# Performance work log

Measured on AMD Instinct MI355X. Metric: run time of the kernel, lower is better.

## Reference

```python
import jax, jax.numpy as jnp
import numpy as np

HIDDEN = 768
HEADS = 12
HEAD_DIM = HIDDEN // HEADS
INTER = 1152
WINDOW = 128
EPS = 1e-5
ROPE_WAVELENGTH = 10000.0


def setup_inputs() -> dict:
    key = jax.random.key(0)
    ks = jax.random.split(key, 8)
    B, S = 2, 2048
    x = jax.random.normal(ks[0], (B, S, HIDDEN), dtype=jnp.float32)
    padding_mask = jnp.ones((B, S), dtype=jnp.int32)
    sc = 0.02
    wqkv = jax.random.normal(ks[1], (HIDDEN, 3 * HIDDEN), dtype=jnp.float32) * sc
    wo_attn = jax.random.normal(ks[2], (HIDDEN, HIDDEN), dtype=jnp.float32) * sc
    wi0 = jax.random.normal(ks[3], (HIDDEN, INTER), dtype=jnp.float32) * sc
    wi1 = jax.random.normal(ks[4], (HIDDEN, INTER), dtype=jnp.float32) * sc
    wo_mlp = jax.random.normal(ks[5], (INTER, HIDDEN), dtype=jnp.float32) * sc
    g_attn = jnp.ones((HIDDEN,), dtype=jnp.float32)
    g_mlp = jnp.ones((HIDDEN,), dtype=jnp.float32)
    return dict(x=x, padding_mask=padding_mask, wqkv=wqkv, wo_attn=wo_attn,
                wi0=wi0, wi1=wi1, wo_mlp=wo_mlp, g_attn=g_attn, g_mlp=g_mlp)


def _rmsnorm(x, gamma):
    # Keras LayerNormalization(rms_scaling=True): x * rsqrt(mean(x^2)+eps) * gamma
    inv = jax.lax.rsqrt(jnp.mean(jnp.square(x), axis=-1, keepdims=True) + EPS)
    return x * inv * gamma


def _rope(t):
    # t: [B, S, H, D]; standard rotate-half RoPE over the head dim
    S, D = t.shape[1], t.shape[3]
    inv_freq = 1.0 / (ROPE_WAVELENGTH ** (jnp.arange(0, D, 2, dtype=jnp.float32) / D))
    freqs = jnp.arange(S, dtype=jnp.float32)[:, None] * inv_freq[None, :]  # [S, D/2]
    emb = jnp.concatenate([freqs, freqs], axis=-1)  # [S, D]
    cos = jnp.cos(emb)[None, :, None, :]
    sin = jnp.sin(emb)[None, :, None, :]
    h1, h2 = jnp.split(t, 2, axis=-1)
    rot = jnp.concatenate([-h2, h1], axis=-1)
    return t * cos + rot * sin


def reference(x, padding_mask, wqkv, wo_attn, wi0, wi1, wo_mlp, g_attn, g_mlp):
    B, S, _ = x.shape
    # --- attention sub-block ---
    res = x
    h = _rmsnorm(x, g_attn)
    qkv = (h @ wqkv).reshape(B, S, 3, HEADS, HEAD_DIM)
    q, k, v = qkv[:, :, 0], qkv[:, :, 1], qkv[:, :, 2]  # [B, S, H, D]
    q = _rope(q)
    k = _rope(k)
    scores = jnp.einsum('bqhd,bkhd->bhqk', q, k) / jnp.sqrt(
        jnp.asarray(HEAD_DIM, x.dtype))
    pos = jnp.arange(S)
    window = (jnp.abs(pos[:, None] - pos[None, :]) <= WINDOW // 2).astype(jnp.float32)
    mask = window[None, None, :, :] * padding_mask.astype(jnp.float32)[:, None, None, :]
    scores = scores + (1.0 - mask) * -1e9
    attn = jax.nn.softmax(scores, axis=-1)
    out = jnp.einsum('bhqk,bkhd->bqhd', attn, v).reshape(B, S, HIDDEN)
    x = res + out @ wo_attn
    # --- GeGLU MLP sub-block ---
    res = x
    h = _rmsnorm(x, g_mlp)
    h = jax.nn.gelu(h @ wi0, approximate=True) * (h @ wi1)
    return res + h @ wo_mlp
```

## Files before the change

### kernel.cpp

```cpp
#include <hip/hip_runtime.h>
#include <hip/hip_bf16.h>

#define HID 768
#define NHEADS 12
#define HD 64
#define INTER 1152
#define SEQ 2048
#define NB 2
#define ROWS (NB * SEQ)
#define QTA 64
#define KTA 192

typedef __attribute__((ext_vector_type(8))) short bf16x8;
typedef __attribute__((ext_vector_type(4))) float f32x4;

__device__ __forceinline__ float bf2f(unsigned short u) {
    union { unsigned int i; float f; } c; c.i = ((unsigned int)u) << 16; return c.f;
}
__device__ __forceinline__ unsigned short f2bf(float f) {
    union { float f; unsigned int i; } c; c.f = f;
    unsigned int b = c.i;
    b += 0x7FFFu + ((b >> 16) & 1u);
    return (unsigned short)(b >> 16);
}
__device__ __forceinline__ void gload16(const void* g, void* l) {
    __builtin_amdgcn_global_load_lds((const __attribute__((address_space(1))) unsigned int*)g,
                                     (__attribute__((address_space(3))) unsigned int*)l,
                                     16, 0, 0);
}

__global__ __launch_bounds__(256) void rmsnorm_kernel(const float* __restrict__ x,
                                                      const float* __restrict__ g,
                                                      unsigned short* __restrict__ out) {
    int row = blockIdx.x;
    const float* xr = x + (size_t)row * HID;
    unsigned short* orow = out + (size_t)row * HID;
    int tid = threadIdx.x;
    float v0 = xr[tid], v1 = xr[tid + 256], v2 = xr[tid + 512];
    float s = v0 * v0 + v1 * v1 + v2 * v2;
    #pragma unroll
    for (int m = 32; m >= 1; m >>= 1) s += __shfl_xor(s, m, 64);
    __shared__ float red[4];
    if ((tid & 63) == 0) red[tid >> 6] = s;
    __syncthreads();
    float tot = red[0] + red[1] + red[2] + red[3];
    float inv = rsqrtf(tot * (1.0f / HID) + 1e-5f);
    orow[tid]       = f2bf(v0 * inv * g[tid]);
    orow[tid + 256] = f2bf(v1 * inv * g[tid + 256]);
    orow[tid + 512] = f2bf(v2 * inv * g[tid + 512]);
}

__device__ __forceinline__ void wt_tile(const float* __restrict__ W,
                                        unsigned short* __restrict__ Wt,
                                        int K, int N, int bx, int by,
                                        float (*t)[33]) {
    int tx = threadIdx.x & 31, ty = threadIdx.x >> 5;
    #pragma unroll
    for (int i = 0; i < 4; ++i)
        t[ty + i * 8][tx] = W[(size_t)(by * 32 + ty + i * 8) * N + bx * 32 + tx];
    __syncthreads();
    #pragma unroll
    for (int i = 0; i < 4; ++i)
        Wt[(size_t)(bx * 32 + ty + i * 8) * K + by * 32 + tx] = f2bf(t[tx][ty + i * 8]);
}

__global__ __launch_bounds__(256) void prep_kernel(const float* __restrict__ wqkv,
                                                   const float* __restrict__ woa,
                                                   const float* __restrict__ wi0,
                                                   const float* __restrict__ wi1,
                                                   const float* __restrict__ wom,
                                                   unsigned short* __restrict__ wqkvT,
                                                   unsigned short* __restrict__ woaT,
                                                   unsigned short* __restrict__ wi0T,
                                                   unsigned short* __restrict__ wi1T,
                                                   unsigned short* __restrict__ womT,
                                                   float2* __restrict__ rtab) {
    __shared__ float t[32][33];
    int id = blockIdx.x;
    if (id < 1728)       wt_tile(wqkv, wqkvT, 768, 2304, id % 72, id / 72, t);
    else if (id < 2304)  { id -= 1728; wt_tile(woa, woaT, 768, 768, id % 24, id / 24, t); }
    else if (id < 3168)  { id -= 2304; wt_tile(wi0, wi0T, 768, 1152, id % 36, id / 36, t); }
    else if (id < 4032)  { id -= 3168; wt_tile(wi1, wi1T, 768, 1152, id % 36, id / 36, t); }
    else if (id < 4896)  { id -= 4032; wt_tile(wom, womT, 1152, 768, id % 24, id / 24, t); }
    else {
        int idx = (id - 4896) * 256 + threadIdx.x;
        int s = idx >> 5, fi = idx & 31;
        float ang = (float)s * exp2f(-(float)fi * 0.41524101186f);
        float sn, cs;
        sincosf(ang, &sn, &cs);
        rtab[idx] = make_float2(cs, sn);
    }
}

__global__ __launch_bounds__(256) void mfma_gemm64(const unsigned short* __restrict__ A,
                                                   const unsigned short* __restrict__ Bt,
                                                   const float* __restrict__ resid,
                                                   float* __restrict__ C,
                                                   int N, int K, int nbx) {
    __shared__ unsigned short As[64 * 64];
    __shared__ unsigned short Bs[64 * 64];
    int nwg = gridDim.x;
    int bid = blockIdx.x;
    int id2 = (bid & 7) * (nwg >> 3) + (bid >> 3);
    int row0 = (id2 / nbx) * 64, col0 = (id2 % nbx) * 64;
    int tid = threadIdx.x;
    int wave = tid >> 6, lane = tid & 63;
    int wr = wave >> 1, wc = wave & 1;
    int fr = lane & 15, fq = lane >> 4;

    f32x4 acc[2][2];
    #pragma unroll
    for (int m = 0; m < 2; ++m)
        #pragma unroll
        for (int n = 0; n < 2; ++n)
            acc[m][n] = (f32x4){0.f, 0.f, 0.f, 0.f};

    const size_t strideA = (size_t)K * 2;
    const char* Ab = (const char*)A;
    const char* Bb = (const char*)Bt;

    for (int k0 = 0; k0 < K; k0 += 64) {
        #pragma unroll
        for (int r = 0; r < 2; ++r) {
            int L = r * 4096 + tid * 16;
            int row = L >> 7;
            int ss = ((L >> 4) & 7) ^ (row & 7);
            gload16(Ab + (size_t)(row0 + row) * strideA + (size_t)k0 * 2 + ss * 16,
                    (char*)As + L);
            gload16(Bb + (size_t)(col0 + row) * strideA + (size_t)k0 * 2 + ss * 16,
                    (char*)Bs + L);
        }
        __syncthreads();
        bf16x8 af[2][2], bff[2][2];
        #pragma unroll
        for (int m = 0; m < 2; ++m)
            #pragma unroll
            for (int kk = 0; kk < 2; ++kk) {
                int rowa = wr * 32 + m * 16 + fr;
                af[m][kk] = *(const bf16x8*)&As[rowa * 64 + ((kk * 4 + fq) ^ (rowa & 7)) * 8];
                int rowb = wc * 32 + m * 16 + fr;
                bff[m][kk] = *(const bf16x8*)&Bs[rowb * 64 + ((kk * 4 + fq) ^ (rowb & 7)) * 8];
            }
        #pragma unroll
        for (int m = 0; m < 2; ++m)
            #pragma unroll
            for (int n = 0; n < 2; ++n) {
                acc[m][n] = __builtin_amdgcn_mfma_f32_16x16x32_bf16(af[m][0], bff[n][0], acc[m][n], 0, 0, 0);
                acc[m][n] = __builtin_amdgcn_mfma_f32_16x16x32_bf16(af[m][1], bff[n][1], acc[m][n], 0, 0, 0);
            }
        __syncthreads();
    }

    #pragma unroll
    for (int m = 0; m < 2; ++m) {
        #pragma unroll
        for (int j = 0; j < 4; ++j) {
            size_t r = (size_t)(row0 + wr * 32 + m * 16 + fq * 4 + j);
            #pragma unroll
            for (int n = 0; n < 2; ++n) {
                size_t idx = r * N + (col0 + wc * 32 + n * 16 + fr);
                float v = acc[m][n][j];
                if (resid) v += resid[idx];
                C[idx] = v;
            }
        }
    }
}

__global__ __launch_bounds__(256) void gemm_qkv128(const unsigned short* __restrict__ A,
                                                   const unsigned short* __restrict__ Bt,
                                                   const float2* __restrict__ rtab,
                                                   unsigned short* __restrict__ Qb,
                                                   unsigned short* __restrict__ Kb,
                                                   unsigned short* __restrict__ Vt) {
    __shared__ unsigned short As[128 * 64];
    __shared__ unsigned short Bs[64 * 64];
    int bid = blockIdx.x;
    int id2 = (bid & 7) * 144 + (bid >> 3);
    int col0 = (id2 % 36) * 64, row0 = (id2 / 36) * 128;
    int tid = threadIdx.x;
    int wave = tid >> 6, lane = tid & 63;
    int fr = lane & 15, fq = lane >> 4;
    int type = col0 / 768;
    int h = (col0 % 768) >> 6;
    int b = row0 >> 11;
    int s0 = row0 & 2047;
    int bh = b * NHEADS + h;

    f32x4 acc[2][4];
    #pragma unroll
    for (int m = 0; m < 2; ++m)
        #pragma unroll
        for (int n = 0; n < 4; ++n)
            acc[m][n] = (f32x4){0.f, 0.f, 0.f, 0.f};

    const size_t strideA = (size_t)768 * 2;
    const char* Ab = (const char*)A;
    const char* Bb = (const char*)Bt;

    for (int k0 = 0; k0 < 768; k0 += 64) {
        #pragma unroll
        for (int r = 0; r < 4; ++r) {
            int L = r * 4096 + tid * 16;
            int row = L >> 7;
            int ss = ((L >> 4) & 7) ^ (row & 7);
            gload16(Ab + (size_t)(row0 + row) * strideA + (size_t)k0 * 2 + ss * 16,
                    (char*)As + L);
        }
        #pragma unroll
        for (int r = 0; r < 2; ++r) {
            int L = r * 4096 + tid * 16;
            int row = L >> 7;
            int ss = ((L >> 4) & 7) ^ (row & 7);
            gload16(Bb + (size_t)(col0 + row) * strideA + (size_t)k0 * 2 + ss * 16,
                    (char*)Bs + L);
        }
        __syncthreads();
        #pragma unroll
        for (int kk = 0; kk < 2; ++kk) {
            bf16x8 af[2], bf[4];
            #pragma unroll
            for (int m = 0; m < 2; ++m) {
                int rowa = wave * 32 + m * 16 + fr;
                af[m] = *(const bf16x8*)&As[rowa * 64 + ((kk * 4 + fq) ^ (rowa & 7)) * 8];
            }
            #pragma unroll
            for (int n = 0; n < 4; ++n) {
                int rowb = n * 16 + fr;
                bf[n] = *(const bf16x8*)&Bs[rowb * 64 + ((kk * 4 + fq) ^ (rowb & 7)) * 8];
            }
            #pragma unroll
            for (int m = 0; m < 2; ++m)
                #pragma unroll
                for (int n = 0; n < 4; ++n)
                    acc[m][n] = __builtin_amdgcn_mfma_f32_16x16x32_bf16(af[m], bf[n], acc[m][n], 0, 0, 0);
        }
        __syncthreads();
    }

    if (type < 2) {
        unsigned short* P = (type == 0 ? Qb : Kb) + ((size_t)bh * SEQ) * 64;
        #pragma unroll
        for (int m = 0; m < 2; ++m)
            #pragma unroll
            for (int n = 0; n < 4; ++n) {
                int d = n * 16 + fr;
                int fi = d & 31;
                #pragma unroll
                for (int j = 0; j < 4; ++j) {
                    int s = s0 + wave * 32 + m * 16 + fq * 4 + j;
                    float2 cs = rtab[s * 32 + fi];
                    float val = acc[m][n][j], par = acc[m][n ^ 2][j];
                    float o = (d < 32) ? val * cs.x - par * cs.y
                                       : val * cs.x + par * cs.y;
                    P[(size_t)s * 64 + d] = f2bf(o);
                }
            }
    } else {
        unsigned short* vt = As;
        #pragma unroll
        for (int m = 0; m < 2; ++m)
            #pragma unroll
            for (int n = 0; n < 4; ++n) {
                int d = n * 16 + fr;
                #pragma unroll
                for (int j = 0; j < 4; ++j)
                    vt[d * 136 + wave * 32 + m * 16 + fq * 4 + j] = f2bf(acc[m][n][j]);
            }
        __syncthreads();
        int d = tid >> 2, sg = tid & 3;
        unsigned short* vrow = Vt + ((size_t)bh * 64 + d) * SEQ + s0 + sg * 32;
        #pragma unroll
        for (int i = 0; i < 4; ++i)
            *(bf16x8*)(vrow + i * 8) = *(const bf16x8*)&vt[d * 136 + sg * 32 + i * 8];
    }
}

__global__ __launch_bounds__(256) void gemm_ffn128(const unsigned short* __restrict__ A,
                                                   const unsigned short* __restrict__ B0t,
                                                   const unsigned short* __restrict__ B1t,
                                                   unsigned short* __restrict__ O) {
    __shared__ unsigned short As[128 * 64];
    __shared__ unsigned short Bs0[64 * 64];
    __shared__ unsigned short Bs1[64 * 64];
    int bid = blockIdx.x;
    int id2 = (bid & 7) * 72 + (bid >> 3);
    int col0 = (id2 % 18) * 64, row0 = (id2 / 18) * 128;
    int tid = threadIdx.x;
    int wave = tid >> 6, lane = tid & 63;
    int fr = lane & 15, fq = lane >> 4;

    f32x4 acc0[2][4], acc1[2][4];
    #pragma unroll
    for (int m = 0; m < 2; ++m)
        #pragma unroll
        for (int n = 0; n < 4; ++n) {
            acc0[m][n] = (f32x4){0.f, 0.f, 0.f, 0.f};
            acc1[m][n] = (f32x4){0.f, 0.f, 0.f, 0.f};
        }

    const size_t strideA = (size_t)768 * 2;
    const char* Ab  = (const char*)A;
    const char* B0b = (const char*)B0t;
    const char* B1b = (const char*)B1t;

    for (int k0 = 0; k0 < 768; k0 += 64) {
        #pragma unroll
        for (int r = 0; r < 4; ++r) {
            int L = r * 4096 + tid * 16;
            int row = L >> 7;
            int ss = ((L >> 4) & 7) ^ (row & 7);
            gload16(Ab + (size_t)(row0 + row) * strideA + (size_t)k0 * 2 + ss * 16,
                    (char*)As + L);
        }
        #pragma unroll
        for (int r = 0; r < 2; ++r) {
            int L = r * 4096 + tid * 16;
            int row = L >> 7;
            int ss = ((L >> 4) & 7) ^ (row & 7);
            size_t goff = (size_t)(col0 + row) * strideA + (size_t)k0 * 2 + ss * 16;
            gload16(B0b + goff, (char*)Bs0 + L);
            gload16(B1b + goff, (char*)Bs1 + L);
        }
        __syncthreads();
        #pragma unroll
        for (int kk = 0; kk < 2; ++kk) {
            bf16x8 af[2], b0[4], b1[4];
            #pragma unroll
            for (int m = 0; m < 2; ++m) {
                int rowa = wave * 32 + m * 16 + fr;
                af[m] = *(const bf16x8*)&As[rowa * 64 + ((kk * 4 + fq) ^ (rowa & 7)) * 8];
            }
            #pragma unroll
            for (int n = 0; n < 4; ++n) {
                int rowb = n * 16 + fr;
                int sl = ((kk * 4 + fq) ^ (rowb & 7)) * 8;
                b0[n] = *(const bf16x8*)&Bs0[rowb * 64 + sl];
                b1[n] = *(const bf16x8*)&Bs1[rowb * 64 + sl];
            }
            #pragma unroll
            for (int m = 0; m < 2; ++m)
                #pragma unroll
                for (int n = 0; n < 4; ++n) {
                    acc0[m][n] = __builtin_amdgcn_mfma_f32_16x16x32_bf16(af[m], b0[n], acc0[m][n], 0, 0, 0);
                    acc1[m][n] = __builtin_amdgcn_mfma_f32_16x16x32_bf16(af[m], b1[n], acc1[m][n], 0, 0, 0);
                }
        }
        __syncthreads();
    }

    #pragma unroll
    for (int m = 0; m < 2; ++m)
        #pragma unroll
        for (int n = 0; n < 4; ++n)
            #pragma unroll
            for (int j = 0; j < 4; ++j) {
                int r = row0 + wave * 32 + m * 16 + fq * 4 + j;
                float xa = acc0[m][n][j];
                float tn = tanhf(0.7978845608028654f * (xa + 0.044715f * xa * xa * xa));
                float gv = 0.5f * xa * (1.f + tn) * acc1[m][n][j];
                O[(size_t)r * INTER + col0 + n * 16 + fr] = f2bf(gv);
            }
}

__global__ __launch_bounds__(256) void attn_mfma(const unsigned short* __restrict__ Qb,
                                                 const unsigned short* __restrict__ Kb,
                                                 const unsigned short* __restrict__ Vt,
                                                 const int* __restrict__ pmask,
                                                 unsigned short* __restrict__ ao) {
    __shared__ unsigned short Ks[KTA * 64];
    __shared__ unsigned short Vs[64 * KTA];
    __shared__ unsigned short Ps[4][16 * KTA];
    __shared__ float pmsk[KTA];

    int bid = blockIdx.x;
    int qt = bid & 31;
    int h  = (bid >> 5) % NHEADS;
    int b  = bid / (32 * NHEADS);
    int bh = b * NHEADS + h;
    int q0 = qt * QTA;
    int kstart = q0 - 64;
    int tid = threadIdx.x;
    int wave = tid >> 6, lane = tid & 63;
    int fr = lane & 15, fq = lane >> 4;

    const unsigned short* Kg = Kb + ((size_t)bh * SEQ) * 64;
    const unsigned short* Vg = Vt + ((size_t)bh * 64) * SEQ;

    if (tid < KTA) {
        int k = kstart + tid;
        pmsk[tid] = (k >= 0 && k < SEQ) ? (1.0f - (float)pmask[b * SEQ + k]) * -1e9f
                                        : -1e9f;
    }

    bool interior = (qt != 0) && (qt != 31);
    if (interior) {
        #pragma unroll
        for (int r = 0; r < 6; ++r) {
            int c = r * 256 + tid;
            int row = c >> 3, slot = c & 7;
            int ss = slot ^ (row & 7);
            gload16(Kg + (size_t)(kstart + row) * 64 + ss * 8, (char*)Ks + c * 16);
        }
        #pragma unroll
        for (int r = 0; r < 6; ++r) {
            int c = r * 256 + tid;
            int d = c / 24, slot = c - d * 24;
            int ss = (slot & ~7) | ((slot & 7) ^ (d & 7));
            gload16(Vg + (size_t)d * SEQ + kstart + ss * 8, (char*)Vs + c * 16);
        }
    } else {
        #pragma unroll
        for (int r = 0; r < 6; ++r) {
            int c = r * 256 + tid;
            int row = c >> 3, slot = c & 7;
            int ss = slot ^ (row & 7);
            int sk = kstart + row;
            bf16x8 val = {0, 0, 0, 0, 0, 0, 0, 0};
            if (sk >= 0 && sk < SEQ)
                val = *(const bf16x8*)(Kg + (size_t)sk * 64 + ss * 8);
            *(bf16x8*)((char*)Ks + c * 16) = val;
        }
        #pragma unroll
        for (int r = 0; r < 6; ++r) {
            int c = r * 256 + tid;
            int d = c / 24, slot = c - d * 24;
            int ss = (slot & ~7) | ((slot & 7) ^ (d & 7));
            int start = kstart + ss * 8;
            bf16x8 val = {0, 0, 0, 0, 0, 0, 0, 0};
            if (start >= 0 && start + 8 <= SEQ)
                val = *(const bf16x8*)(Vg + (size_t)d * SEQ + start);
            *(bf16x8*)((char*)Vs + c * 16) = val;
        }
    }
    __syncthreads();

    const unsigned short* Qg = Qb + ((size_t)bh * SEQ + q0 + wave * 16 + fr) * 64 + fq * 8;
    bf16x8 qf0 = *(const bf16x8*)(Qg);
    bf16x8 qf1 = *(const bf16x8*)(Qg + 32);

    f32x4 sc[12];
    #pragma unroll
    for (int n = 0; n < 12; ++n) sc[n] = (f32x4){0.f, 0.f, 0.f, 0.f};
    #pragma unroll
    for (int n = 0; n < 12; ++n) {
        int row = n * 16 + fr;
        int base = row * 64;
        bf16x8 k0 = *(const bf16x8*)&Ks[base + ((fq)     ^ (row & 7)) * 8];
        bf16x8 k1 = *(const bf16x8*)&Ks[base + ((4 + fq) ^ (row & 7)) * 8];
        sc[n] = __builtin_amdgcn_mfma_f32_16x16x32_bf16(qf0, k0, sc[n], 0, 0, 0);
        sc[n] = __builtin_amdgcn_mfma_f32_16x16x32_bf16(qf1, k1, sc[n], 0, 0, 0);
    }

    int qrow_base = q0 + wave * 16 + fq * 4;
    float mj[4] = {-1e30f, -1e30f, -1e30f, -1e30f}, sj[4];
    #pragma unroll
    for (int n = 0; n < 12; ++n) {
        int k = kstart + n * 16 + fr;
        float pm = pmsk[n * 16 + fr];
        #pragma unroll
        for (int j = 0; j < 4; ++j) {
            int diff = qrow_base + j - k;
            float s = sc[n][j] * 0.125f + pm;
            if (diff > 64 || diff < -64) s = -1e30f;
            sc[n][j] = s;
            mj[j] = fmaxf(mj[j], s);
        }
    }
    #pragma unroll
    for (int j = 0; j < 4; ++j) {
        #pragma unroll
        for (int mk = 1; mk < 16; mk <<= 1)
            mj[j] = fmaxf(mj[j], __shfl_xor(mj[j], mk, 16));
        sj[j] = 0.f;
    }
    #pragma unroll
    for (int n = 0; n < 12; ++n)
        #pragma unroll
        for (int j = 0; j < 4; ++j) {
            float e = expf(sc[n][j] - mj[j]);
            sc[n][j] = e;
            sj[j] += e;
        }
    #pragma unroll
    for (int j = 0; j < 4; ++j)
        #pragma unroll
        for (int mk = 1; mk < 16; mk <<= 1)
            sj[j] += __shfl_xor(sj[j], mk, 16);

    unsigned short* Pw = Ps[wave];
    #pragma unroll
    for (int n = 0; n < 12; ++n) {
        int slot = n * 2 + (fr >> 3);
        #pragma unroll
        for (int j = 0; j < 4; ++j) {
            int row = fq * 4 + j;
            int ss = (slot & ~7) | ((slot & 7) ^ (row & 7));
            Pw[row * KTA + ss * 8 + (fr & 7)] = f2bf(sc[n][j]);
        }
    }

    f32x4 oacc[4];
    #pragma unroll
    for (int n = 0; n < 4; ++n) oacc[n] = (f32x4){0.f, 0.f, 0.f, 0.f};
    #pragma unroll
    for (int kt = 0; kt < 6; ++kt) {
        int slot = kt * 4 + fq;
        int ssp = (slot & ~7) | ((slot & 7) ^ (fr & 7));
        bf16x8 pa = *(const bf16x8*)&Pw[fr * KTA + ssp * 8];
        #pragma unroll
        for (int n = 0; n < 4; ++n) {
            int d = n * 16 + fr;
            int ssv = (slot & ~7) | ((slot & 7) ^ (d & 7));
            bf16x8 vf = *(const bf16x8*)&Vs[d * KTA + ssv * 8];
            oacc[n] = __builtin_amdgcn_mfma_f32_16x16x32_bf16(pa, vf, oacc[n], 0, 0, 0);
        }
    }

    unsigned short* aob = ao + ((size_t)(b * SEQ + qrow_base)) * HID + h * 64;
    float rs[4];
    #pragma unroll
    for (int j = 0; j < 4; ++j) rs[j] = 1.0f / sj[j];
    #pragma unroll
    for (int n = 0; n < 4; ++n)
        #pragma unroll
        for (int j = 0; j < 4; ++j)
            aob[(size_t)j * HID + n * 16 + fr] = f2bf(oacc[n][j] * rs[j]);
}

extern "C" void kernel_launch(void* const* d_in, const int* in_sizes, int n_in,
                              void* d_out, int out_size, void* d_ws, size_t ws_size,
                              hipStream_t stream) {
    const float* x       = (const float*)d_in[0];
    const int*   pmask   = (const int*)d_in[1];
    const float* wqkv    = (const float*)d_in[2];
    const float* wo_attn = (const float*)d_in[3];
    const float* wi0     = (const float*)d_in[4];
    const float* wi1     = (const float*)d_in[5];
    const float* wo_mlp  = (const float*)d_in[6];
    const float* g_attn  = (const float*)d_in[7];
    const float* g_mlp   = (const float*)d_in[8];
    float* out = (float*)d_out;

    char* w = (char*)d_ws;
    unsigned short* hbf   = (unsigned short*)(w);
    unsigned short* aobf  = (unsigned short*)(w + 6291456);
    unsigned short* Qb    = (unsigned short*)(w + 12582912);
    unsigned short* Kb    = (unsigned short*)(w + 18874368);
    unsigned short* Vt    = (unsigned short*)(w + 25165824);
    unsigned short* mgate = (unsigned short*)(w + 31457280);
    float2*         rtab  = (float2*)(w + 40894464);
    unsigned short* wqkvT = (unsigned short*)(w + 41418752);
    unsigned short* woaT  = (unsigned short*)(w + 44957696);
    unsigned short* wi0T  = (unsigned short*)(w + 46137344);
    unsigned short* wi1T  = (unsigned short*)(w + 47906816);
    unsigned short* womT  = (unsigned short*)(w + 49676288);

    prep_kernel<<<5152, 256, 0, stream>>>(wqkv, wo_attn, wi0, wi1, wo_mlp,
                                          wqkvT, woaT, wi0T, wi1T, womT, rtab);
    rmsnorm_kernel<<<ROWS, 256, 0, stream>>>(x, g_attn, hbf);
    gemm_qkv128<<<1152, 256, 0, stream>>>(hbf, wqkvT, rtab, Qb, Kb, Vt);
    attn_mfma<<<NB * NHEADS * (SEQ / QTA), 256, 0, stream>>>(Qb, Kb, Vt, pmask, aobf);
    mfma_gemm64<<<768, 256, 0, stream>>>(aobf, woaT, x, out, 768, 768, 12);
    rmsnorm_kernel<<<ROWS, 256, 0, stream>>>(out, g_mlp, hbf);
    gemm_ffn128<<<576, 256, 0, stream>>>(hbf, wi0T, wi1T, mgate);
    mfma_gemm64<<<768, 256, 0, stream>>>(mgate, womT, out, out, 768, 1152, 12);
}
```

Measured before the change: 128.3 us.

## Double-buffer LDS tiles in GEMM kernels and hoist Q loads in attention

The three MFMA GEMM kernels (generic, QKV, GeGLU) now use two LDS buffers, issuing the next K-tile's global-to-LDS loads before computing on the current tile. This is meant to overlap global memory latency with MFMA work. In the attention kernel, the Q fragment loads move ahead of the K/V staging and barrier so their latency overlaps. LDS usage doubles, which may reduce occupancy, especially for the GeGLU kernel.

```diff
diff --git a/kernel.cpp b/kernel.cpp
--- a/kernel.cpp
+++ b/kernel.cpp
@@ -97,8 +97,8 @@
                                                    const float* __restrict__ resid,
                                                    float* __restrict__ C,
                                                    int N, int K, int nbx) {
-    __shared__ unsigned short As[64 * 64];
-    __shared__ unsigned short Bs[64 * 64];
+    __shared__ unsigned short As[2 * 64 * 64];
+    __shared__ unsigned short Bs[2 * 64 * 64];
     int nwg = gridDim.x;
     int bid = blockIdx.x;
     int id2 = (bid & 7) * (nwg >> 3) + (bid >> 3);
@@ -108,38 +108,47 @@
     int wr = wave >> 1, wc = wave & 1;
     int fr = lane & 15, fq = lane >> 4;
 
-    f32x4 acc[2][2];
-    #pragma unroll
-    for (int m = 0; m < 2; ++m)
-        #pragma unroll
-        for (int n = 0; n < 2; ++n)
-            acc[m][n] = (f32x4){0.f, 0.f, 0.f, 0.f};
-
     const size_t strideA = (size_t)K * 2;
     const char* Ab = (const char*)A;
     const char* Bb = (const char*)Bt;
 
-    for (int k0 = 0; k0 < K; k0 += 64) {
+    auto stage = [&](int buf, int k0) {
         #pragma unroll
         for (int r = 0; r < 2; ++r) {
             int L = r * 4096 + tid * 16;
             int row = L >> 7;
             int ss = ((L >> 4) & 7) ^ (row & 7);
             gload16(Ab + (size_t)(row0 + row) * strideA + (size_t)k0 * 2 + ss * 16,
-                    (char*)As + L);
+                    (char*)As + buf * 8192 + L);
             gload16(Bb + (size_t)(col0 + row) * strideA + (size_t)k0 * 2 + ss * 16,
-                    (char*)Bs + L);
-        }
-        __syncthreads();
+                    (char*)Bs + buf * 8192 + L);
+        }
+    };
+
+    f32x4 acc[2][2];
+    #pragma unroll
+    for (int m = 0; m < 2; ++m)
+        #pragma unroll
+        for (int n = 0; n < 2; ++n)
+            acc[m][n] = (f32x4){0.f, 0.f, 0.f, 0.f};
+
+    stage(0, 0);
+    __syncthreads();
+    int nt = K >> 6;
+    for (int t = 0; t < nt; ++t) {
+        int cur = t & 1;
+        if (t + 1 < nt) stage(cur ^ 1, (t + 1) << 6);
+        const unsigned short* Asb = As + cur * 4096;
+        const unsigned short* Bsb = Bs + cur * 4096;
         bf16x8 af[2][2], bff[2][2];
         #pragma unroll
         for (int m = 0; m < 2; ++m)
             #pragma unroll
             for (int kk = 0; kk < 2; ++kk) {
                 int rowa = wr * 32 + m * 16 + fr;
-                af[m][kk] = *(const bf16x8*)&As[rowa * 64 + ((kk * 4 + fq) ^ (rowa & 7)) * 8];
+                af[m][kk] = *(const bf16x8*)&Asb[rowa * 64 + ((kk * 4 + fq) ^ (rowa & 7)) * 8];
                 int rowb = wc * 32 + m * 16 + fr;
-                bff[m][kk] = *(const bf16x8*)&Bs[rowb * 64 + ((kk * 4 + fq) ^ (rowb & 7)) * 8];
+                bff[m][kk] = *(const bf16x8*)&Bsb[rowb * 64 + ((kk * 4 + fq) ^ (rowb & 7)) * 8];
             }
         #pragma unroll
         for (int m = 0; m < 2; ++m)
@@ -173,8 +182,8 @@
                                                    unsigned short* __restrict__ Qb,
                                                    unsigned short* __restrict__ Kb,
                                                    unsigned short* __restrict__ Vt) {
-    __shared__ unsigned short As[128 * 64];
-    __shared__ unsigned short Bs[64 * 64];
+    __shared__ unsigned short As[2 * 128 * 64];
+    __shared__ unsigned short Bs[2 * 64 * 64];
     int bid = blockIdx.x;
     int id2 = (bid & 7) * 144 + (bid >> 3);
     int col0 = (id2 % 36) * 64, row0 = (id2 / 36) * 128;
@@ -187,25 +196,18 @@
     int s0 = row0 & 2047;
     int bh = b * NHEADS + h;
 
-    f32x4 acc[2][4];
-    #pragma unroll
-    for (int m = 0; m < 2; ++m)
-        #pragma unroll
-        for (int n = 0; n < 4; ++n)
-            acc[m][n] = (f32x4){0.f, 0.f, 0.f, 0.f};
-
     const size_t strideA = (size_t)768 * 2;
     const char* Ab = (const char*)A;
     const char* Bb = (const char*)Bt;
 
-    for (int k0 = 0; k0 < 768; k0 += 64) {
+    auto stage = [&](int buf, int k0) {
         #pragma unroll
         for (int r = 0; r < 4; ++r) {
             int L = r * 4096 + tid * 16;
             int row = L >> 7;
             int ss = ((L >> 4) & 7) ^ (row & 7);
             gload16(Ab + (size_t)(row0 + row) * strideA + (size_t)k0 * 2 + ss * 16,
-                    (char*)As + L);
+                    (char*)As + buf * 16384 + L);
         }
         #pragma unroll
         for (int r = 0; r < 2; ++r) {
@@ -213,21 +215,36 @@
             int row = L >> 7;
             int ss = ((L >> 4) & 7) ^ (row & 7);
             gload16(Bb + (size_t)(col0 + row) * strideA + (size_t)k0 * 2 + ss * 16,
-                    (char*)Bs + L);
-        }
-        __syncthreads();
+                    (char*)Bs + buf * 8192 + L);
+        }
+    };
+
+    f32x4 acc[2][4];
+    #pragma unroll
+    for (int m = 0; m < 2; ++m)
+        #pragma unroll
+        for (int n = 0; n < 4; ++n)
+            acc[m][n] = (f32x4){0.f, 0.f, 0.f, 0.f};
+
+    stage(0, 0);
+    __syncthreads();
+    for (int t = 0; t < 12; ++t) {
+        int cur = t & 1;
+        if (t < 11) stage(cur ^ 1, (t + 1) << 6);
+        const unsigned short* Asb = As + cur * 8192;
+        const unsigned short* Bsb = Bs + cur * 4096;
         #pragma unroll
         for (int kk = 0; kk < 2; ++kk) {
             bf16x8 af[2], bf[4];
             #pragma unroll
             for (int m = 0; m < 2; ++m) {
                 int rowa = wave * 32 + m * 16 + fr;
-                af[m] = *(const bf16x8*)&As[rowa * 64 + ((kk * 4 + fq) ^ (rowa & 7)) * 8];
+                af[m] = *(const bf16x8*)&Asb[rowa * 64 + ((kk * 4 + fq) ^ (rowa & 7)) * 8];
             }
             #pragma unroll
             for (int n = 0; n < 4; ++n) {
                 int rowb = n * 16 + fr;
-                bf[n] = *(const bf16x8*)&Bs[rowb * 64 + ((kk * 4 + fq) ^ (rowb & 7)) * 8];
+                bf[n] = *(const bf16x8*)&Bsb[rowb * 64 + ((kk * 4 + fq) ^ (rowb & 7)) * 8];
             }
             #pragma unroll
             for (int m = 0; m < 2; ++m)
@@ -280,9 +297,9 @@
                                                    const unsigned short* __restrict__ B0t,
                                                    const unsigned short* __restrict__ B1t,
                                                    unsigned short* __restrict__ O) {
-    __shared__ unsigned short As[128 * 64];
-    __shared__ unsigned short Bs0[64 * 64];
-    __shared__ unsigned short Bs1[64 * 64];
+    __shared__ unsigned short As[2 * 128 * 64];
+    __shared__ unsigned short Bs0[2 * 64 * 64];
+    __shared__ unsigned short Bs1[2 * 64 * 64];
     int bid = blockIdx.x;
     int id2 = (bid & 7) * 72 + (bid >> 3);
     int col0 = (id2 % 18) * 64, row0 = (id2 / 18) * 128;
@@ -290,28 +307,19 @@
     int wave = tid >> 6, lane = tid & 63;
     int fr = lane & 15, fq = lane >> 4;
 
-    f32x4 acc0[2][4], acc1[2][4];
-    #pragma unroll
-    for (int m = 0; m < 2; ++m)
-        #pragma unroll
-        for (int n = 0; n < 4; ++n) {
-            acc0[m][n] = (f32x4){0.f, 0.f, 0.f, 0.f};
-            acc1[m][n] = (f32x4){0.f, 0.f, 0.f, 0.f};
-        }
-
     const size_t strideA = (size_t)768 * 2;
     const char* Ab  = (const char*)A;
     const char* B0b = (const char*)B0t;
     const char* B1b = (const char*)B1t;
 
-    for (int k0 = 0; k0 < 768; k0 += 64) {
+    auto stage = [&](int buf, int k0) {
         #pragma unroll
         for (int r = 0; r < 4; ++r) {
             int L = r * 4096 + tid * 16;
             int row = L >> 7;
             int ss = ((L >> 4) & 7) ^ (row & 7);
             gload16(Ab + (size_t)(row0 + row) * strideA + (size_t)k0 * 2 + ss * 16,
-                    (char*)As + L);
+                    (char*)As + buf * 16384 + L);
         }
         #pragma unroll
         for (int r = 0; r < 2; ++r) {
@@ -319,24 +327,42 @@
             int row = L >> 7;
             int ss = ((L >> 4) & 7) ^ (row & 7);
             size_t goff = (size_t)(col0 + row) * strideA + (size_t)k0 * 2 + ss * 16;
-            gload16(B0b + goff, (char*)Bs0 + L);
-            gload16(B1b + goff, (char*)Bs1 + L);
-        }
-        __syncthreads();
+            gload16(B0b + goff, (char*)Bs0 + buf * 8192 + L);
+            gload16(B1b + goff, (char*)Bs1 + buf * 8192 + L);
+        }
+    };
+
+    f32x4 acc0[2][4], acc1[2][4];
+    #pragma unroll
+    for (int m = 0; m < 2; ++m)
+        #pragma unroll
+        for (int n = 0; n < 4; ++n) {
+            acc0[m][n] = (f32x4){0.f, 0.f, 0.f, 0.f};
+            acc1[m][n] = (f32x4){0.f, 0.f, 0.f, 0.f};
+        }
+
+    stage(0, 0);
+    __syncthreads();
+    for (int t = 0; t < 12; ++t) {
+        int cur = t & 1;
+        if (t < 11) stage(cur ^ 1, (t + 1) << 6);
+        const unsigned short* Asb  = As  + cur * 8192;
+        const unsigned short* Bs0b = Bs0 + cur * 4096;
+        const unsigned short* Bs1b = Bs1 + cur * 4096;
         #pragma unroll
         for (int kk = 0; kk < 2; ++kk) {
             bf16x8 af[2], b0[4], b1[4];
             #pragma unroll
             for (int m = 0; m < 2; ++m) {
                 int rowa = wave * 32 + m * 16 + fr;
-                af[m] = *(const bf16x8*)&As[rowa * 64 + ((kk * 4 + fq) ^ (rowa & 7)) * 8];
+                af[m] = *(const bf16x8*)&Asb[rowa * 64 + ((kk * 4 + fq) ^ (rowa & 7)) * 8];
             }
             #pragma unroll
             for (int n = 0; n < 4; ++n) {
                 int rowb = n * 16 + fr;
                 int sl = ((kk * 4 + fq) ^ (rowb & 7)) * 8;
-                b0[n] = *(const bf16x8*)&Bs0[rowb * 64 + sl];
-                b1[n] = *(const bf16x8*)&Bs1[rowb * 64 + sl];
+                b0[n] = *(const bf16x8*)&Bs0b[rowb * 64 + sl];
+                b1[n] = *(const bf16x8*)&Bs1b[rowb * 64 + sl];
             }
             #pragma unroll
             for (int m = 0; m < 2; ++m)
@@ -387,6 +413,9 @@
     const unsigned short* Kg = Kb + ((size_t)bh * SEQ) * 64;
     const unsigned short* Vg = Vt + ((size_t)bh * 64) * SEQ;
 
+    const unsigned short* Qg = Qb + ((size_t)bh * SEQ + q0 + wave * 16 + fr) * 64 + fq * 8;
+    bf16x8 qf0 = *(const bf16x8*)(Qg);
+    bf16x8 qf1 = *(const bf16x8*)(Qg + 32);
     if (tid < KTA) {
         int k = kstart + tid;
         pmsk[tid] = (k >= 0 && k < SEQ) ? (1.0f - (float)pmask[b * SEQ + k]) * -1e9f
@@ -434,10 +463,6 @@
         }
     }
     __syncthreads();
-
-    const unsigned short* Qg = Qb + ((size_t)bh * SEQ + q0 + wave * 16 + fr) * 64 + fq * 8;
-    bf16x8 qf0 = *(const bf16x8*)(Qg);
-    bf16x8 qf1 = *(const bf16x8*)(Qg + 32);
 
     f32x4 sc[12];
     #pragma unroll
```

Result: slower. 140.2 us (+9.3%).
